# Performance work log

Measured on AMD Instinct MI355X. Metric: run time of the kernel, lower is better.

The kernel has to match this reference:

```python
import jax, jax.numpy as jnp
import numpy as np

B, N, D, K = 4, 4096, 128, 20

def setup_inputs() -> dict:
    key = jax.random.key(0)
    k1, k2, k3 = jax.random.split(key, 3)
    s = 1.0 / np.sqrt(D)
    return {
        "x": jax.random.normal(k1, (B, N, D), dtype=jnp.float32),
        "Wq": jax.random.normal(k2, (D, D), dtype=jnp.float32) * s,
        "bq": jnp.zeros((D,), dtype=jnp.float32),
        "Wk": jax.random.normal(k3, (D, D), dtype=jnp.float32) * s,
        "bk": jnp.zeros((D,), dtype=jnp.float32),
    }

def reference(x, Wq, bq, Wk, bk):
    # Q/K projections: [B,N,D]
    Q = jnp.einsum('bnd,de->bne', x, Wq) + bq
    Kp = jnp.einsum('bnd,de->bne', x, Wk) + bk
    # scores: [B,N,N], scaled by sqrt(D)
    attn = jnp.einsum('bnd,bmd->bnm', Q, Kp) / jnp.sqrt(jnp.float32(D))
    # top-k along last dim -> binary mask via scatter
    _, topk_idx = jax.lax.top_k(attn, K)  # [B,N,K]
    bi = jnp.arange(B)[:, None, None]
    ni = jnp.arange(N)[None, :, None]
    mask = jnp.zeros_like(attn).at[bi, ni, topk_idx].set(1.0)
    # zero out non-topk entries, then full softmax over all N (zeros included,
    # matching the torch module exactly)
    sparse_attn = attn * mask
    out = jax.nn.softmax(sparse_attn, axis=-1)
    return out[..., None]  # [B,N,N,1]
```

## Files before the change

### kernel.cpp

```cpp
#include <hip/hip_runtime.h>

#define BN 4096
#define BD 128
#define NB 4
#define TOPK 20
#define CAND 128
#define EPS 0.06f

typedef float f32x16 __attribute__((ext_vector_type(16)));
typedef short bf16x8 __attribute__((ext_vector_type(8)));

__device__ inline unsigned short f2bf(float f) {
  unsigned int u = __float_as_uint(f);
  unsigned int r = (u + 0x7FFFu + ((u >> 16) & 1u)) >> 16;
  return (unsigned short)r;
}

__global__ __launch_bounds__(256) void proj_kernel(
    const float* __restrict__ x,
    const float* __restrict__ Wq, const float* __restrict__ bq,
    const float* __restrict__ Wk, const float* __restrict__ bk,
    double* __restrict__ Qd, double* __restrict__ Kd, unsigned short* __restrict__ Khi) {
  __shared__ double xs[32][129];
  const int tid = threadIdx.x;
  const long row0 = (long)blockIdx.x * 32;
  const float* xsrc = x + row0 * BD;
  for (int i = tid; i < 32 * BD; i += 256) xs[i >> 7][i & 127] = (double)xsrc[i];
  __syncthreads();

  const int e = tid & 127;
  const bool isK = tid >= 128;
  const float* W = isK ? Wk : Wq;
  const float* bias = isK ? bk : bq;
  double* Od = isK ? Kd : Qd;

  double acc[32];
  const double binit = (double)bias[e];
#pragma unroll
  for (int r = 0; r < 32; ++r) acc[r] = binit;

  for (int d = 0; d < BD; ++d) {
    const double wv = (double)W[d * BD + e];
#pragma unroll
    for (int r = 0; r < 32; ++r) acc[r] = fma(xs[r][d], wv, acc[r]);
  }

#pragma unroll
  for (int r = 0; r < 32; ++r) {
    const double a = acc[r];
    const long o = (row0 + r) * BD + e;
    Od[o] = a;
    if (isK) Khi[o] = f2bf((float)a);
  }
}

__global__ __launch_bounds__(512) void screen_kernel(
    const double* __restrict__ Qd, const unsigned short* __restrict__ Khi,
    unsigned short* __restrict__ cand, unsigned int* __restrict__ cnt) {
  __shared__ char kbuf[32768];
  __shared__ unsigned short pool[64][24];
  __shared__ float tauLds[64];
  __shared__ unsigned int scnt[64];
  __shared__ unsigned short slist[64][CAND];

  const int tid = threadIdx.x;
  const int lane = tid & 63;
  const int w = tid >> 6;
  const int kt = w & 3, qt = w >> 2;
  const int c31 = lane & 31, hi = lane >> 5;
  const int blk = blockIdx.x;
  const int b = (blk & 7) >> 1;
  const int ib = ((blk >> 3) << 1) | (blk & 1);
  const int rowbase = ib << 6;
  const int qrow = qt * 32 + c31;
  const float RS = 0.088388347648318447f;

  bf16x8 bqf[8];
  {
    const double* qp = Qd + ((long)b * BN + rowbase + qrow) * BD + hi * 8;
#pragma unroll
    for (int ks = 0; ks < 8; ++ks) {
      bf16x8 pk;
#pragma unroll
      for (int j = 0; j < 8; ++j) pk[j] = (short)f2bf((float)qp[ks * 16 + j]);
      bqf[ks] = pk;
    }
  }

  const char* kb = (const char*)(Khi + (long)b * BN * BD);
  const int ar = kt * 32 + c31;
  const int ar256 = ar * 256;
  const int ar7 = ar & 7;

  uint4 stg[4];
#define LOADSTG(s)                                              \
  do {                                                          \
    const char* gsrc_ = kb + (long)(s)*32768 + tid * 16;        \
    stg[0] = *(const uint4*)(gsrc_);                            \
    stg[1] = *(const uint4*)(gsrc_ + 8192);                     \
    stg[2] = *(const uint4*)(gsrc_ + 16384);                    \
    stg[3] = *(const uint4*)(gsrc_ + 24576);                    \
  } while (0)
#define WRITESTG()                                              \
  do {                                                          \
    _Pragma("unroll") for (int j_ = 0; j_ < 4; ++j_) {          \
      const int L_ = j_ * 8192 + tid * 16;                      \
      const int r_ = L_ >> 8;                                   \
      const int c_ = (L_ >> 4) & 15;                            \
      *(uint4*)(kbuf + r_ * 256 + ((c_ ^ (r_ & 7)) << 4)) = stg[j_]; \
    }                                                           \
  } while (0)

  LOADSTG(0);
  WRITESTG();
  __syncthreads();

  float t1 = -3.4e38f, t2 = -3.4e38f, t3 = -3.4e38f;
  for (int step = 0; step < 32; ++step) {
    if (step < 31) LOADSTG(step + 1);
    f32x16 acc = {0.f, 0.f, 0.f, 0.f, 0.f, 0.f, 0.f, 0.f,
                  0.f, 0.f, 0.f, 0.f, 0.f, 0.f, 0.f, 0.f};
#pragma unroll
    for (int ks = 0; ks < 8; ++ks) {
      const bf16x8 a = *(const bf16x8*)(kbuf + ar256 + (((ks * 2 + hi) ^ ar7) << 4));
      acc = __builtin_amdgcn_mfma_f32_32x32x16_bf16(a, bqf[ks], acc, 0, 0, 0);
    }
#pragma unroll
    for (int reg = 0; reg < 16; ++reg) {
      const float s = acc[reg] * RS;
      const float w1 = fmaxf(t1, s), l1 = fminf(t1, s);
      const float w2 = fmaxf(t2, l1), l2 = fminf(t2, l1);
      t3 = fmaxf(t3, l2);
      t2 = w2;
      t1 = w1;
    }
    __syncthreads();
    if (step < 31) WRITESTG();
    __syncthreads();
  }

  {
    const int cid = kt * 2 + hi;
    pool[qrow][cid * 3 + 0] = (unsigned short)(__float_as_uint(t1) >> 16);
    pool[qrow][cid * 3 + 1] = (unsigned short)(__float_as_uint(t2) >> 16);
    pool[qrow][cid * 3 + 2] = (unsigned short)(__float_as_uint(t3) >> 16);
  }
  if (tid < 64) scnt[tid] = 0;
  __syncthreads();

  for (int it2 = 0; it2 < 4; ++it2) {
    const int row = w * 8 + it2 * 2 + hi;
    float v = (c31 < 24) ? __uint_as_float((unsigned int)pool[row][c31] << 16) : -3.4e38f;
#pragma unroll
    for (int k = 2; k <= 32; k <<= 1) {
#pragma unroll
      for (int j = k >> 1; j > 0; j >>= 1) {
        const float o = __shfl_xor(v, j);
        const bool keepmin = (((c31 & k) == 0) == ((c31 & j) == 0));
        v = keepmin ? fminf(v, o) : fmaxf(v, o);
      }
    }
    if (c31 == 12) tauLds[row] = v;
  }
  __syncthreads();

  const float th = tauLds[qrow] - EPS;

  LOADSTG(0);
  WRITESTG();
  __syncthreads();

  for (int step = 0; step < 32; ++step) {
    if (step < 31) LOADSTG(step + 1);
    f32x16 acc = {0.f, 0.f, 0.f, 0.f, 0.f, 0.f, 0.f, 0.f,
                  0.f, 0.f, 0.f, 0.f, 0.f, 0.f, 0.f, 0.f};
#pragma unroll
    for (int ks = 0; ks < 8; ++ks) {
      const bf16x8 a = *(const bf16x8*)(kbuf + ar256 + (((ks * 2 + hi) ^ ar7) << 4));
      acc = __builtin_amdgcn_mfma_f32_32x32x16_bf16(a, bqf[ks], acc, 0, 0, 0);
    }
#pragma unroll
    for (int reg = 0; reg < 16; ++reg) {
      const float s = acc[reg] * RS;
      if (s >= th) {
        const int kv = step * 128 + kt * 32 + ((reg & 3) + 8 * (reg >> 2) + 4 * hi);
        unsigned int p = atomicAdd(&scnt[qrow], 1u);
        if (p < CAND) slist[qrow][p] = (unsigned short)kv;
      }
    }
    __syncthreads();
    if (step < 31) WRITESTG();
    __syncthreads();
  }

  const long growbase = (long)b * BN + rowbase;
  if (tid < 64) cnt[growbase + tid] = min(scnt[tid], (unsigned int)CAND);
  const unsigned short* sl = &slist[0][0];
  for (int j = tid; j < 64 * CAND; j += 512) cand[growbase * CAND + j] = sl[j];
#undef LOADSTG
#undef WRITESTG
}

__device__ inline float rescore_f64(const double2* __restrict__ kp2, const double2* __restrict__ q2) {
  double a0 = 0.0, a1 = 0.0, a2 = 0.0, a3 = 0.0;
#pragma unroll
  for (int i = 0; i < 64; i += 4) {
    a0 = fma(q2[i + 0].y, kp2[i + 0].y, fma(q2[i + 0].x, kp2[i + 0].x, a0));
    a1 = fma(q2[i + 1].y, kp2[i + 1].y, fma(q2[i + 1].x, kp2[i + 1].x, a1));
    a2 = fma(q2[i + 2].y, kp2[i + 2].y, fma(q2[i + 2].x, kp2[i + 2].x, a2));
    a3 = fma(q2[i + 3].y, kp2[i + 3].y, fma(q2[i + 3].x, kp2[i + 3].x, a3));
  }
  return (float)(((a0 + a1) + (a2 + a3)) * 8.8388347648318447e-02);
}

__device__ inline unsigned int fmono(float v) {
  const unsigned int u = __float_as_uint(v);
  return (u & 0x80000000u) ? ~u : (u | 0x80000000u);
}
__device__ inline float fdemono(unsigned int k) {
  const unsigned int u = (k & 0x80000000u) ? (k & 0x7fffffffu) : ~k;
  return __uint_as_float(u);
}

__global__ __launch_bounds__(256) void finalize_kernel(
    const double* __restrict__ Qd, const double* __restrict__ Kd,
    const unsigned short* __restrict__ cand, const unsigned int* __restrict__ cnt,
    float* __restrict__ out) {
  const int tid = threadIdx.x;
  const int lane = tid & 63;
  const int w = tid >> 6;
  const int blk = blockIdx.x;
  const int b = (blk & 7) >> 1;
  const int idx = ((blk >> 3) << 1) | (blk & 1);
  const long row = (long)b * BN + idx * 4 + w;
  float* outrow = out + row * BN;
  const double* kb = Kd + (long)b * BN * BD;
  const double2* q2 = (const double2*)(Qd + row * BD);

  const int c = (int)min(cnt[row], (unsigned int)CAND);

  unsigned long long key0 = 0ull, key1 = 0ull;
  if (lane < c) {
    const int kv = (int)cand[row * CAND + lane];
    const float v = rescore_f64((const double2*)(kb + (long)kv * BD), q2);
    key0 = ((unsigned long long)fmono(v) << 12) | (unsigned int)(4095 - kv);
  }
  if (lane + 64 < c) {
    const int kv = (int)cand[row * CAND + lane + 64];
    const float v = rescore_f64((const double2*)(kb + (long)kv * BD), q2);
    key1 = ((unsigned long long)fmono(v) << 12) | (unsigned int)(4095 - kv);
  }
  if (key1 > key0) { const unsigned long long t = key0; key0 = key1; key1 = t; }

  float m = 0.0f, se = 0.0f;
  float myval = 0.0f;
  int mycol = 0;
  for (int it = 0; it < TOPK; ++it) {
    unsigned long long rk = key0;
    for (int off = 32; off; off >>= 1) {
      const unsigned long long ok = __shfl_xor(rk, off);
      rk = (ok > rk) ? ok : rk;
    }
    const float rv = fdemono((unsigned int)(rk >> 12));
    if (it == 0) m = fmaxf(rv, 0.0f);
    se += expf(rv - m);
    if (lane == it) { myval = rv; mycol = 4095 - (int)(rk & 0xFFFull); }
    if (key0 == rk) { key0 = key1; key1 = 0ull; }
  }

  const float Z = se + (float)(BN - TOPK) * expf(-m);
  const float c0 = expf(-m) / Z;

  const float4 cv = make_float4(c0, c0, c0, c0);
  float4* op = (float4*)outrow;
#pragma unroll
  for (int i = 0; i < 16; ++i) op[i * 64 + lane] = cv;

  asm volatile("s_waitcnt vmcnt(0)" ::: "memory");
  if (lane < TOPK) outrow[mycol] = expf(myval - m) / Z;
}

extern "C" void kernel_launch(void* const* d_in, const int* in_sizes, int n_in,
                              void* d_out, int out_size, void* d_ws, size_t ws_size,
                              hipStream_t stream) {
  const float* x  = (const float*)d_in[0];
  const float* Wq = (const float*)d_in[1];
  const float* bq = (const float*)d_in[2];
  const float* Wk = (const float*)d_in[3];
  const float* bk = (const float*)d_in[4];
  float* out = (float*)d_out;

  const long NE = (long)NB * BN * BD;
  double* Qd = (double*)d_ws;
  double* Kd = Qd + NE;
  unsigned short* Khi = (unsigned short*)(Kd + NE);
  unsigned short* cand = Khi + NE;
  unsigned int* cnt = (unsigned int*)(cand + (long)NB * BN * CAND);

  proj_kernel<<<NB * BN / 32, 256, 0, stream>>>(x, Wq, bq, Wk, bk, Qd, Kd, Khi);
  screen_kernel<<<NB * (BN / 64), 512, 0, stream>>>(Qd, Khi, cand, cnt);
  finalize_kernel<<<NB * (BN / 4), 256, 0, stream>>>(Qd, Kd, cand, cnt, out);
}
```

Baseline: 389.2 us.

## Split screening across key-quarter blocks with separate tau pass and double-buffered LDS

The single screen kernel is split in two, each launched over 1024 blocks. Every block now covers one 1024-key quarter for 64 query rows, where before one block swept all 4096 keys. A new tau kernel merges the per-quarter top-2 candidates (64 per row) with a bitonic sort to set the threshold, and the second screening pass writes up to 48 candidates per quarter, which finalize rescored as up to 3 keys per lane. The K tile staging is double-buffered in LDS, dropping one barrier per step, and the XOR swizzle widens to 16. This exposes 4x more blocks and should raise parallelism, at the cost of extra launches, a recomputed Q fragment per block, and a changed candidate-capture heuristic (top-2 per 32-key chunk instead of top-3) that could miss true top-k entries.

```diff
diff --git a/kernel.cpp b/kernel.cpp
--- a/kernel.cpp
+++ b/kernel.cpp
@@ -4,7 +4,8 @@
 #define BD 128
 #define NB 4
 #define TOPK 20
-#define CAND 128
+#define CAP 48
+#define SLOTS 192
 #define EPS 0.06f
 
 typedef float f32x16 __attribute__((ext_vector_type(16)));
@@ -54,151 +55,151 @@
   }
 }
 
-__global__ __launch_bounds__(512) void screen_kernel(
+template <int MODE>
+__global__ __launch_bounds__(512) void screen_kernel_t(
     const double* __restrict__ Qd, const unsigned short* __restrict__ Khi,
-    unsigned short* __restrict__ cand, unsigned int* __restrict__ cnt) {
-  __shared__ char kbuf[32768];
-  __shared__ unsigned short pool[64][24];
-  __shared__ float tauLds[64];
-  __shared__ unsigned int scnt[64];
-  __shared__ unsigned short slist[64][CAND];
+    unsigned int* __restrict__ poolG, const float* __restrict__ tauG,
+    unsigned short* __restrict__ slistG, unsigned int* __restrict__ cnt4G) {
+  __shared__ char kbuf[2][32768];
+  __shared__ unsigned int scnt[MODE ? 64 : 1];
+  __shared__ unsigned short slist[MODE ? 64 : 1][CAP];
 
   const int tid = threadIdx.x;
   const int lane = tid & 63;
   const int w = tid >> 6;
   const int kt = w & 3, qt = w >> 2;
   const int c31 = lane & 31, hi = lane >> 5;
+
   const int blk = blockIdx.x;
-  const int b = (blk & 7) >> 1;
-  const int ib = ((blk >> 3) << 1) | (blk & 1);
-  const int rowbase = ib << 6;
+  const int xcd = blk & 7;
+  const int j = blk >> 3;
+  const int combo = xcd * 2 + (j & 1);
+  const int b = combo >> 2;
+  const int kq = combo & 3;
+  const int rg = j >> 1;
+  const int rowbase = rg << 6;
+  const int kvbase = kq << 10;
+
   const int qrow = qt * 32 + c31;
+  const long grow = (long)b * BN + rowbase + qrow;
   const float RS = 0.088388347648318447f;
 
   bf16x8 bqf[8];
   {
-    const double* qp = Qd + ((long)b * BN + rowbase + qrow) * BD + hi * 8;
+    const double* qp = Qd + grow * BD + hi * 8;
 #pragma unroll
     for (int ks = 0; ks < 8; ++ks) {
       bf16x8 pk;
 #pragma unroll
-      for (int j = 0; j < 8; ++j) pk[j] = (short)f2bf((float)qp[ks * 16 + j]);
+      for (int jj = 0; jj < 8; ++jj) pk[jj] = (short)f2bf((float)qp[ks * 16 + jj]);
       bqf[ks] = pk;
     }
   }
 
-  const char* kb = (const char*)(Khi + (long)b * BN * BD);
+  float th = 0.0f;
+  if constexpr (MODE == 1) {
+    th = tauG[grow];
+    if (tid < 64) scnt[tid] = 0;
+  }
+
+  const char* kb = (const char*)(Khi + ((long)b * BN + kvbase) * BD);
   const int ar = kt * 32 + c31;
   const int ar256 = ar * 256;
-  const int ar7 = ar & 7;
+  const int arx = ar & 15;
 
   uint4 stg[4];
-#define LOADSTG(s)                                              \
-  do {                                                          \
-    const char* gsrc_ = kb + (long)(s)*32768 + tid * 16;        \
-    stg[0] = *(const uint4*)(gsrc_);                            \
-    stg[1] = *(const uint4*)(gsrc_ + 8192);                     \
-    stg[2] = *(const uint4*)(gsrc_ + 16384);                    \
-    stg[3] = *(const uint4*)(gsrc_ + 24576);                    \
-  } while (0)
-#define WRITESTG()                                              \
-  do {                                                          \
-    _Pragma("unroll") for (int j_ = 0; j_ < 4; ++j_) {          \
-      const int L_ = j_ * 8192 + tid * 16;                      \
-      const int r_ = L_ >> 8;                                   \
-      const int c_ = (L_ >> 4) & 15;                            \
-      *(uint4*)(kbuf + r_ * 256 + ((c_ ^ (r_ & 7)) << 4)) = stg[j_]; \
-    }                                                           \
-  } while (0)
+#define LOADSTG(s)                                                \
+  {                                                               \
+    const char* gsrc_ = kb + (long)(s)*32768 + tid * 16;          \
+    stg[0] = *(const uint4*)(gsrc_);                              \
+    stg[1] = *(const uint4*)(gsrc_ + 8192);                       \
+    stg[2] = *(const uint4*)(gsrc_ + 16384);                      \
+    stg[3] = *(const uint4*)(gsrc_ + 24576);                      \
+  }
+#define WRITESTG(pp)                                              \
+  {                                                               \
+    char* base_ = kbuf[pp];                                       \
+    _Pragma("unroll") for (int j_ = 0; j_ < 4; ++j_) {            \
+      const int L_ = j_ * 8192 + tid * 16;                        \
+      const int r_ = L_ >> 8;                                     \
+      const int c_ = (L_ >> 4) & 15;                              \
+      *(uint4*)(base_ + r_ * 256 + ((c_ ^ (r_ & 15)) << 4)) = stg[j_]; \
+    }                                                             \
+  }
+
+  float t1 = -3.4e38f, t2 = -3.4e38f;
 
   LOADSTG(0);
-  WRITESTG();
+  WRITESTG(0);
   __syncthreads();
 
-  float t1 = -3.4e38f, t2 = -3.4e38f, t3 = -3.4e38f;
-  for (int step = 0; step < 32; ++step) {
-    if (step < 31) LOADSTG(step + 1);
+  for (int step = 0; step < 8; ++step) {
+    const int p = step & 1;
+    if (step < 7) LOADSTG(step + 1);
+
     f32x16 acc = {0.f, 0.f, 0.f, 0.f, 0.f, 0.f, 0.f, 0.f,
                   0.f, 0.f, 0.f, 0.f, 0.f, 0.f, 0.f, 0.f};
 #pragma unroll
     for (int ks = 0; ks < 8; ++ks) {
-      const bf16x8 a = *(const bf16x8*)(kbuf + ar256 + (((ks * 2 + hi) ^ ar7) << 4));
+      const bf16x8 a = *(const bf16x8*)(kbuf[p] + ar256 + (((ks * 2 + hi) ^ arx) << 4));
       acc = __builtin_amdgcn_mfma_f32_32x32x16_bf16(a, bqf[ks], acc, 0, 0, 0);
     }
+
 #pragma unroll
     for (int reg = 0; reg < 16; ++reg) {
       const float s = acc[reg] * RS;
-      const float w1 = fmaxf(t1, s), l1 = fminf(t1, s);
-      const float w2 = fmaxf(t2, l1), l2 = fminf(t2, l1);
-      t3 = fmaxf(t3, l2);
-      t2 = w2;
-      t1 = w1;
-    }
+      if constexpr (MODE == 0) {
+        const float w1 = fmaxf(t1, s);
+        t2 = fmaxf(t2, fminf(t1, s));
+        t1 = w1;
+      } else {
+        if (s >= th) {
+          const int kv = kvbase + step * 128 + kt * 32 + ((reg & 3) + 8 * (reg >> 2) + 4 * hi);
+          const unsigned int pidx = atomicAdd(&scnt[qrow], 1u);
+          if (pidx < CAP) slist[qrow][pidx] = (unsigned short)kv;
+        }
+      }
+    }
+
+    if (step < 7) WRITESTG(p ^ 1);
     __syncthreads();
-    if (step < 31) WRITESTG();
-    __syncthreads();
-  }
-
-  {
-    const int cid = kt * 2 + hi;
-    pool[qrow][cid * 3 + 0] = (unsigned short)(__float_as_uint(t1) >> 16);
-    pool[qrow][cid * 3 + 1] = (unsigned short)(__float_as_uint(t2) >> 16);
-    pool[qrow][cid * 3 + 2] = (unsigned short)(__float_as_uint(t3) >> 16);
-  }
-  if (tid < 64) scnt[tid] = 0;
-  __syncthreads();
-
-  for (int it2 = 0; it2 < 4; ++it2) {
-    const int row = w * 8 + it2 * 2 + hi;
-    float v = (c31 < 24) ? __uint_as_float((unsigned int)pool[row][c31] << 16) : -3.4e38f;
-#pragma unroll
-    for (int k = 2; k <= 32; k <<= 1) {
-#pragma unroll
-      for (int j = k >> 1; j > 0; j >>= 1) {
-        const float o = __shfl_xor(v, j);
-        const bool keepmin = (((c31 & k) == 0) == ((c31 & j) == 0));
-        v = keepmin ? fminf(v, o) : fmaxf(v, o);
-      }
-    }
-    if (c31 == 12) tauLds[row] = v;
-  }
-  __syncthreads();
-
-  const float th = tauLds[qrow] - EPS;
-
-  LOADSTG(0);
-  WRITESTG();
-  __syncthreads();
-
-  for (int step = 0; step < 32; ++step) {
-    if (step < 31) LOADSTG(step + 1);
-    f32x16 acc = {0.f, 0.f, 0.f, 0.f, 0.f, 0.f, 0.f, 0.f,
-                  0.f, 0.f, 0.f, 0.f, 0.f, 0.f, 0.f, 0.f};
-#pragma unroll
-    for (int ks = 0; ks < 8; ++ks) {
-      const bf16x8 a = *(const bf16x8*)(kbuf + ar256 + (((ks * 2 + hi) ^ ar7) << 4));
-      acc = __builtin_amdgcn_mfma_f32_32x32x16_bf16(a, bqf[ks], acc, 0, 0, 0);
-    }
-#pragma unroll
-    for (int reg = 0; reg < 16; ++reg) {
-      const float s = acc[reg] * RS;
-      if (s >= th) {
-        const int kv = step * 128 + kt * 32 + ((reg & 3) + 8 * (reg >> 2) + 4 * hi);
-        unsigned int p = atomicAdd(&scnt[qrow], 1u);
-        if (p < CAND) slist[qrow][p] = (unsigned short)kv;
-      }
-    }
-    __syncthreads();
-    if (step < 31) WRITESTG();
-    __syncthreads();
-  }
-
-  const long growbase = (long)b * BN + rowbase;
-  if (tid < 64) cnt[growbase + tid] = min(scnt[tid], (unsigned int)CAND);
-  const unsigned short* sl = &slist[0][0];
-  for (int j = tid; j < 64 * CAND; j += 512) cand[growbase * CAND + j] = sl[j];
+  }
+
+  if constexpr (MODE == 0) {
+    const unsigned int pk =
+        ((__float_as_uint(t2) >> 16) << 16) | (__float_as_uint(t1) >> 16);
+    poolG[grow * 32 + kq * 8 + kt * 2 + hi] = pk;
+  } else {
+    if (tid < 64) cnt4G[((long)b * BN + rowbase + tid) * 4 + kq] = min(scnt[tid], (unsigned int)CAP);
+    for (int i = tid; i < 64 * CAP; i += 512) {
+      const int r = i / CAP, c = i - (i / CAP) * CAP;
+      slistG[((long)b * BN + rowbase + r) * SLOTS + kq * CAP + c] = slist[r][c];
+    }
+  }
 #undef LOADSTG
 #undef WRITESTG
+}
+
+__global__ __launch_bounds__(512) void tau_kernel(
+    const unsigned int* __restrict__ poolG, float* __restrict__ tauG) {
+  const int tid = threadIdx.x;
+  const int lane = tid & 63;
+  const int w = tid >> 6;
+  const long row = (long)blockIdx.x * 8 + w;
+
+  const unsigned int pv = poolG[row * 32 + (lane >> 1)];
+  float v = __uint_as_float((lane & 1) ? (pv & 0xFFFF0000u) : (pv << 16));
+
+#pragma unroll
+  for (int k = 2; k <= 64; k <<= 1) {
+#pragma unroll
+    for (int jj = k >> 1; jj > 0; jj >>= 1) {
+      const float o = __shfl_xor(v, jj);
+      const bool keepmin = (((lane & k) == 0) == ((lane & jj) == 0));
+      v = keepmin ? fminf(v, o) : fmaxf(v, o);
+    }
+  }
+  if (lane == 44) tauG[row] = v - EPS;
 }
 
 __device__ inline float rescore_f64(const double2* __restrict__ kp2, const double2* __restrict__ q2) {
@@ -224,7 +225,7 @@
 
 __global__ __launch_bounds__(256) void finalize_kernel(
     const double* __restrict__ Qd, const double* __restrict__ Kd,
-    const unsigned short* __restrict__ cand, const unsigned int* __restrict__ cnt,
+    const unsigned short* __restrict__ slistG, const unsigned int* __restrict__ cnt4G,
     float* __restrict__ out) {
   const int tid = threadIdx.x;
   const int lane = tid & 63;
@@ -237,19 +238,27 @@
   const double* kb = Kd + (long)b * BN * BD;
   const double2* q2 = (const double2*)(Qd + row * BD);
 
-  const int c = (int)min(cnt[row], (unsigned int)CAND);
-
-  unsigned long long key0 = 0ull, key1 = 0ull;
-  if (lane < c) {
-    const int kv = (int)cand[row * CAND + lane];
-    const float v = rescore_f64((const double2*)(kb + (long)kv * BD), q2);
-    key0 = ((unsigned long long)fmono(v) << 12) | (unsigned int)(4095 - kv);
-  }
-  if (lane + 64 < c) {
-    const int kv = (int)cand[row * CAND + lane + 64];
-    const float v = rescore_f64((const double2*)(kb + (long)kv * BD), q2);
-    key1 = ((unsigned long long)fmono(v) << 12) | (unsigned int)(4095 - kv);
-  }
+  const uint4 c4 = *(const uint4*)(cnt4G + row * 4);
+
+  unsigned long long key0 = 0ull, key1 = 0ull, key2 = 0ull;
+#pragma unroll
+  for (int t = 0; t < 3; ++t) {
+    const int s = lane + t * 64;
+    const int q = s / CAP;
+    const int i = s - q * CAP;
+    const unsigned int cq = (q & 1) ? ((q & 2) ? c4.w : c4.y) : ((q & 2) ? c4.z : c4.x);
+    if ((unsigned int)i < cq) {
+      const int kv = (int)slistG[row * SLOTS + s];
+      const float v = rescore_f64((const double2*)(kb + (long)kv * BD), q2);
+      const unsigned long long kk =
+          ((unsigned long long)fmono(v) << 12) | (unsigned int)(4095 - kv);
+      if (t == 0) key0 = kk;
+      else if (t == 1) key1 = kk;
+      else key2 = kk;
+    }
+  }
+  if (key1 > key0) { const unsigned long long t = key0; key0 = key1; key1 = t; }
+  if (key2 > key1) { const unsigned long long t = key1; key1 = key2; key2 = t; }
   if (key1 > key0) { const unsigned long long t = key0; key0 = key1; key1 = t; }
 
   float m = 0.0f, se = 0.0f;
@@ -265,7 +274,7 @@
     if (it == 0) m = fmaxf(rv, 0.0f);
     se += expf(rv - m);
     if (lane == it) { myval = rv; mycol = 4095 - (int)(rk & 0xFFFull); }
-    if (key0 == rk) { key0 = key1; key1 = 0ull; }
+    if (key0 == rk) { key0 = key1; key1 = key2; key2 = 0ull; }
   }
 
   const float Z = se + (float)(BN - TOPK) * expf(-m);
@@ -294,10 +303,14 @@
   double* Qd = (double*)d_ws;
   double* Kd = Qd + NE;
   unsigned short* Khi = (unsigned short*)(Kd + NE);
-  unsigned short* cand = Khi + NE;
-  unsigned int* cnt = (unsigned int*)(cand + (long)NB * BN * CAND);
+  unsigned short* slistG = Khi + NE;
+  unsigned int* poolG = (unsigned int*)slistG;
+  unsigned int* cnt4G = (unsigned int*)(slistG + (long)NB * BN * SLOTS);
+  float* tauG = (float*)(cnt4G + (long)NB * BN * 4);
 
   proj_kernel<<<NB * BN / 32, 256, 0, stream>>>(x, Wq, bq, Wk, bk, Qd, Kd, Khi);
-  screen_kernel<<<NB * (BN / 64), 512, 0, stream>>>(Qd, Khi, cand, cnt);
-  finalize_kernel<<<NB * (BN / 4), 256, 0, stream>>>(Qd, Kd, cand, cnt, out);
-}
+  screen_kernel_t<0><<<1024, 512, 0, stream>>>(Qd, Khi, poolG, nullptr, nullptr, nullptr);
+  tau_kernel<<<NB * BN / 8, 512, 0, stream>>>(poolG, tauG);
+  screen_kernel_t<1><<<1024, 512, 0, stream>>>(Qd, Khi, nullptr, tauG, slistG, cnt4G);
+  finalize_kernel<<<NB * BN / 4, 256, 0, stream>>>(Qd, Kd, slistG, cnt4G, out);
+}
```

After: 413.6 us. 1.06x slower.
